# Performance work log

Measured on AMD Instinct MI355X. Metric: run time of the kernel, lower is better.

## Reference

```python
import jax, jax.numpy as jnp
import numpy as np

T, N, E = 4, 40000, 640000
D_IN, D_HID, D_OUT, NCLASS = 256, 256, 256, 2
NEG = 0.2  # leaky_relu negative slope (both GATv2 internal and outer activations)


def segment_softmax(logits, seg, n):
    m = jax.ops.segment_max(logits, seg, num_segments=n)
    ex = jnp.exp(logits - m[seg])
    s = jax.ops.segment_sum(ex, seg, num_segments=n)
    return ex / s[seg]


def gatv2(x, src, dst, Wl, Wr, bl, br, att, bias, n):
    # PyG GATv2Conv, heads=1, concat: lin_l on source, lin_r on target,
    # e = att . leaky_relu(xl_j + xr_i), softmax over incoming edges of i,
    # out_i = sum_j alpha_ij * xl_j + bias. Self-loops already appended.
    xl = x @ Wl + bl                                   # [n, C]
    xr = x @ Wr + br                                   # [n, C]
    e = jax.nn.leaky_relu(xl[src] + xr[dst], NEG)      # [E', C]
    alpha = segment_softmax(e @ att, dst, n)           # [E']
    out = jax.ops.segment_sum(alpha[:, None] * xl[src], dst, num_segments=n)
    return out + bias


def setup_inputs() -> dict:
    key = jax.random.key(0)
    ks = jax.random.split(key, 18)
    w = lambda k, shape, fan: (jax.random.normal(k, shape, dtype=jnp.float32) / np.sqrt(fan)).astype(jnp.float32)
    return {
        "fts": jax.random.normal(ks[0], (T, N, D_IN), dtype=jnp.float32),
        "graph": jax.random.randint(ks[1], (T, 2, E), 0, N, dtype=jnp.int32),
        "Wl0": w(ks[2], (D_IN, D_HID), D_IN),
        "Wr0": w(ks[3], (D_IN, D_HID), D_IN),
        "bl0": jnp.zeros((D_HID,), jnp.float32),
        "br0": jnp.zeros((D_HID,), jnp.float32),
        "att0": w(ks[4], (D_HID,), D_HID),
        "b0": jnp.zeros((D_HID,), jnp.float32),
        "Wl1": w(ks[5], (D_HID, D_OUT), D_HID),
        "Wr1": w(ks[6], (D_HID, D_OUT), D_HID),
        "bl1": jnp.zeros((D_OUT,), jnp.float32),
        "br1": jnp.zeros((D_OUT,), jnp.float32),
        "att1": w(ks[7], (D_OUT,), D_OUT),
        "b1": jnp.zeros((D_OUT,), jnp.float32),
        "W_lin": w(ks[8], (D_OUT, NCLASS), D_OUT),
        "b_lin": jnp.zeros((NCLASS,), jnp.float32),
        "time_steps": T,
    }


def reference(fts, graph, Wl0, Wr0, bl0, br0, att0, b0,
              Wl1, Wr1, bl1, br1, att1, b1, W_lin, b_lin, time_steps):
    n = fts.shape[1]
    loops = jnp.arange(n, dtype=graph.dtype)
    # PyG add_self_loops=True: append (i, i) edges per graph used.
    src0 = jnp.concatenate([graph[0, 0], loops])
    dst0 = jnp.concatenate([graph[0, 1], loops])
    # BUG-faithful: only timestep 0 survives (y = y[0]) but the last layer
    # uses G from the LAST timestep; timesteps 1..T-1 are dead compute.
    srcL = jnp.concatenate([graph[time_steps - 1, 0], loops])
    dstL = jnp.concatenate([graph[time_steps - 1, 1], loops])
    y = jax.nn.leaky_relu(gatv2(fts[0], src0, dst0, Wl0, Wr0, bl0, br0, att0, b0, n), NEG)
    y = jax.nn.leaky_relu(gatv2(y, srcL, dstL, Wl1, Wr1, bl1, br1, att1, b1, n), NEG)
    # dropout is identity in eval mode
    y = y @ W_lin + b_lin
    return jax.nn.log_softmax(y, axis=1)  # [N, nclass]
```

## Files before the change

### kernel.cpp

```cpp
#include <hip/hip_runtime.h>
#include <hip/hip_bf16.h>
#include <math.h>

#define NEG 0.2f
#define NB_MAX 256
#define CAP 5120

typedef float f32x4 __attribute__((ext_vector_type(4)));
typedef _Float16 f16;
typedef _Float16 f16x2 __attribute__((ext_vector_type(2)));
typedef _Float16 f16x8 __attribute__((ext_vector_type(8)));

#if defined(__has_builtin)
#if __has_builtin(__builtin_amdgcn_fdot2)
#define HAVE_FDOT2 1
#endif
#endif

typedef __attribute__((address_space(3))) void as3_void;
typedef __attribute__((address_space(1))) const void as1_void;

__device__ __forceinline__ void gl_lds16(const void* g, void* l) {
    __builtin_amdgcn_global_load_lds((as1_void*)g, (as3_void*)l, 16, 0, 0);
}

__global__ __launch_bounds__(256) void convert_w2(const float* __restrict__ Wl0,
                                                  const float* __restrict__ Wr0,
                                                  const float* __restrict__ Wl1,
                                                  const float* __restrict__ Wr1,
                                                  _Float16* __restrict__ Wt,
                                                  int* __restrict__ bkt_next, int nb2) {
    int l = blockIdx.y;
    int idx = blockIdx.x * blockDim.x + threadIdx.x;
    int n = idx >> 8, k = idx & 255;
    const float* Wl = l ? Wl1 : Wl0;
    const float* Wr = l ? Wr1 : Wr0;
    float v = (n < 256) ? Wl[k * 256 + n] : Wr[k * 256 + (n - 256)];
    Wt[(size_t)l * 512 * 256 + idx] = (_Float16)v;
    if (blockIdx.x == 0 && l == 0)
        for (int i = threadIdx.x; i < nb2; i += 256) bkt_next[i] = 0;
}

__device__ __forceinline__ void stage16(const _Float16* __restrict__ src,
                                        int row_base, int row_max, int k0,
                                        char* lds, int tid) {
#pragma unroll
    for (int q = 0; q < 2; ++q) {
        int off = q * 4096 + tid * 16;
        int row = off >> 6;
        int slot = (off >> 4) & 3;
        int se = slot ^ (row & 3);
        int grow = row_base + row;
        if (grow > row_max) grow = row_max;
        gl_lds16(src + (size_t)grow * 256 + k0 + se * 8,
                 lds + q * 4096 + (tid >> 6) * 1024);
    }
}

__device__ __forceinline__ void stage16_f32(const float* __restrict__ X,
                                            int row_base, int row_max, int k0,
                                            char* lds, int tid) {
#pragma unroll
    for (int u = 0; u < 4; ++u) {
        int unit = u * 256 + tid;
        int r = unit >> 3, hu = unit & 7;
        int slot = hu >> 1, sub = (hu & 1) * 8;
        int se = slot ^ (r & 3);
        int grow = row_base + r;
        if (grow > row_max) grow = row_max;
        float4 v = *(const float4*)(X + (size_t)grow * 256 + k0 + se * 8 + (hu & 1) * 4);
        f16x2 p0 = {(f16)v.x, (f16)v.y};
        f16x2 p1 = {(f16)v.z, (f16)v.w};
        uint2 w;
        w.x = __builtin_bit_cast(unsigned, p0);
        w.y = __builtin_bit_cast(unsigned, p1);
        *(uint2*)(lds + r * 64 + slot * 16 + sub) = w;
    }
}

template <int SRC>
__global__ __launch_bounds__(256) void mfma_gemm(const float* __restrict__ Xf,
                                                 const _Float16* __restrict__ X16,
                                                 const _Float16* __restrict__ Wt,
                                                 const float* __restrict__ bl,
                                                 const float* __restrict__ br,
                                                 _Float16* __restrict__ Af,
                                                 _Float16* __restrict__ Bf, int M) {
    __shared__ char smem[32768];
    int Mb = (M + 127) >> 7;
    int b = blockIdx.x;
    int cx = b & 7, rr = b >> 3;
    int m_blk = (rr >> 2) * 8 + cx;
    int n_blk = rr & 3;
    if (m_blk >= Mb) return;
    int tid = threadIdx.x;
    int wave = tid >> 6, lane = tid & 63;
    int m0 = m_blk * 128;
    int wr = wave >> 1, wc = wave & 1;
    int r15 = lane & 15, c = lane >> 4;

    f32x4 acc[4][4];
#pragma unroll
    for (int mf = 0; mf < 4; ++mf)
#pragma unroll
        for (int nf = 0; nf < 4; ++nf) acc[mf][nf] = (f32x4){0.f, 0.f, 0.f, 0.f};

    auto stageX = [&](int k0, char* dst) {
        if constexpr (SRC == 0) stage16_f32(Xf, m0, M - 1, k0, dst, tid);
        else                    stage16(X16, m0, M - 1, k0, dst, tid);
    };

    stageX(0, smem);
    stage16(Wt, n_blk * 128, 511, 0, smem + 8192, tid);
    __syncthreads();

    for (int t = 0; t < 8; ++t) {
        int buf = t & 1;
        if (t < 7) {
            char* nb = smem + (buf ^ 1) * 16384;
            stageX((t + 1) * 32, nb);
            stage16(Wt, n_blk * 128, 511, (t + 1) * 32, nb + 8192, tid);
        }
        const char* At = smem + buf * 16384;
        const char* Bt = At + 8192;
        f16x8 af[4], bf[4];
#pragma unroll
        for (int f = 0; f < 4; ++f) {
            int ar = wr * 64 + f * 16 + r15;
            af[f] = *(const f16x8*)(At + ar * 64 + ((c ^ (ar & 3)) << 4));
            int br_ = wc * 64 + f * 16 + r15;
            bf[f] = *(const f16x8*)(Bt + br_ * 64 + ((c ^ (br_ & 3)) << 4));
        }
#pragma unroll
        for (int mf = 0; mf < 4; ++mf)
#pragma unroll
            for (int nf = 0; nf < 4; ++nf)
                acc[mf][nf] = __builtin_amdgcn_mfma_f32_16x16x32_f16(af[mf], bf[nf], acc[mf][nf], 0, 0, 0);
        __syncthreads();
    }

    int q4 = (lane >> 4) * 4;
#pragma unroll
    for (int nf = 0; nf < 4; ++nf) {
        int n_abs = n_blk * 128 + wc * 64 + nf * 16 + r15;
        bool left = n_abs < 256;
        float bb = left ? bl[n_abs] : br[n_abs - 256];
        int col = n_abs & 255;
#pragma unroll
        for (int mf = 0; mf < 4; ++mf) {
            int rowb = m0 + wr * 64 + mf * 16 + q4;
#pragma unroll
            for (int j = 0; j < 4; ++j) {
                int row = rowb + j;
                if (row < M) {
                    float v = acc[mf][nf][j] + bb;
                    if (left) Af[(size_t)row * 256 + col] = (_Float16)v;
                    else      Bf[(size_t)row * 256 + col] = (_Float16)v;
                }
            }
        }
    }
}

__global__ __launch_bounds__(256) void binA(const int* __restrict__ src0,
                                            const int* __restrict__ dst0,
                                            const int* __restrict__ src1,
                                            const int* __restrict__ dst1,
                                            int Ereal, int EP, int nb,
                                            int* __restrict__ bkt_next,
                                            unsigned* __restrict__ bucketBuf) {
    __shared__ int hist[NB_MAX], base[NB_MAX], ofs[NB_MAX];
    int l = blockIdx.y;
    for (int i = threadIdx.x; i < nb; i += 256) hist[i] = 0;
    __syncthreads();
    const int* src = l ? src1 : src0;
    const int* dst = l ? dst1 : dst0;
    int c0 = blockIdx.x * 4096;
    int dcache[16];
#pragma unroll
    for (int k = 0; k < 16; ++k) {
        int i = c0 + k * 256 + threadIdx.x;
        int d = -1;
        if (i < EP) d = (i < Ereal) ? dst[i] : (i - Ereal);
        dcache[k] = d;
        if (d >= 0) atomicAdd(&hist[d >> 8], 1);
    }
    __syncthreads();
    for (int i = threadIdx.x; i < nb; i += 256) {
        base[i] = hist[i] ? atomicAdd(&bkt_next[l * nb + i], hist[i]) : 0;
        ofs[i] = 0;
    }
    __syncthreads();
#pragma unroll
    for (int k = 0; k < 16; ++k) {
        int i = c0 + k * 256 + threadIdx.x;
        int d = dcache[k];
        if (d >= 0) {
            int s = (i < Ereal) ? src[i] : (i - Ereal);
            int bk = d >> 8;
            int pos = base[bk] + atomicAdd(&ofs[bk], 1);
            bucketBuf[(size_t)(l * nb + bk) * CAP + pos] = (unsigned)s | ((unsigned)(d & 255) << 16);
        }
    }
}

__global__ __launch_bounds__(256) void binB(const unsigned* __restrict__ bucketBuf,
                                            const int* __restrict__ bkt_cnt,
                                            int nb, int N,
                                            int* __restrict__ beg,
                                            int* __restrict__ end_,
                                            int* __restrict__ csr) {
    __shared__ int hist[256], sh[256], nxt[256];
    int b = blockIdx.x, l = blockIdx.y, t = threadIdx.x;
    int cnt = bkt_cnt[l * nb + b];
    const unsigned* buf = bucketBuf + (size_t)(l * nb + b) * CAP;
    int* csrL = csr + (size_t)l * nb * CAP;
    hist[t] = 0;
    __syncthreads();
    for (int i = t; i < cnt; i += 256)
        atomicAdd(&hist[buf[i] >> 16], 1);
    __syncthreads();
    int h = hist[t];
    sh[t] = h;
    __syncthreads();
    for (int o = 1; o < 256; o <<= 1) {
        int x = (t >= o) ? sh[t - o] : 0;
        __syncthreads();
        sh[t] += x;
        __syncthreads();
    }
    int excl = sh[t] - h;
    nxt[t] = excl;
    int d = b * 256 + t;
    if (d < N) {
        beg[(size_t)l * N + d] = b * CAP + excl;
        end_[(size_t)l * N + d] = b * CAP + excl + h;
    }
    __syncthreads();
    for (int i = t; i < cnt; i += 256) {
        unsigned v = buf[i];
        int pos = b * CAP + atomicAdd(&nxt[v >> 16], 1);
        csrL[pos] = (int)(v & 0xFFFFu);
    }
}

template <int MODE>
__global__ __launch_bounds__(256) void gat_node(const _Float16* __restrict__ xl,
                                                const _Float16* __restrict__ xr,
                                                const int* __restrict__ beg_,
                                                const int* __restrict__ end_,
                                                const int* __restrict__ csr_src,
                                                const float* __restrict__ att,
                                                const float* __restrict__ bias,
                                                _Float16* __restrict__ y16,
                                                const float* __restrict__ Wlin,
                                                const float* __restrict__ blin,
                                                float* __restrict__ out, int n) {
    int wid = (int)((blockIdx.x * (size_t)blockDim.x + threadIdx.x) >> 6);
    int lane = threadIdx.x & 63;
    if (wid >= n) return;
    int g = lane >> 5, li = lane & 31;
    int beg = beg_[wid], end = end_[wid];

    f16x8 xr8 = ((const f16x8*)(xr + (size_t)wid * 256))[li];
    float4 t0 = ((const float4*)att)[li * 2];
    float4 t1 = ((const float4*)att)[li * 2 + 1];
    f16x2 t01 = {(f16)t0.x, (f16)t0.y}, t23 = {(f16)t0.z, (f16)t0.w};
    f16x2 t45 = {(f16)t1.x, (f16)t1.y}, t67 = {(f16)t1.z, (f16)t1.w};
    const f16 ng = (f16)NEG;
    const f16x8 n8 = {ng, ng, ng, ng, ng, ng, ng, ng};

    float m = -INFINITY, ssum = 0.f;
    float acc[8] = {0.f, 0.f, 0.f, 0.f, 0.f, 0.f, 0.f, 0.f};

    auto step = [&](f16x8 a, bool valid) {
        f16x8 v = a + xr8;
        f16x8 lk = __builtin_elementwise_max(v, v * n8);
#ifdef HAVE_FDOT2
        f16x2 q;
        q[0] = lk[0]; q[1] = lk[1];
        float dot = __builtin_amdgcn_fdot2(q, t01, 0.f, false);
        q[0] = lk[2]; q[1] = lk[3];
        dot = __builtin_amdgcn_fdot2(q, t23, dot, false);
        q[0] = lk[4]; q[1] = lk[5];
        dot = __builtin_amdgcn_fdot2(q, t45, dot, false);
        q[0] = lk[6]; q[1] = lk[7];
        dot = __builtin_amdgcn_fdot2(q, t67, dot, false);
#else
        float dot = (float)lk[0] * (float)t01[0] + (float)lk[1] * (float)t01[1] +
                    (float)lk[2] * (float)t23[0] + (float)lk[3] * (float)t23[1] +
                    (float)lk[4] * (float)t45[0] + (float)lk[5] * (float)t45[1] +
                    (float)lk[6] * (float)t67[0] + (float)lk[7] * (float)t67[1];
#endif
#pragma unroll
        for (int off = 16; off > 0; off >>= 1) dot += __shfl_xor(dot, off);
        if (valid) {
            if (dot > m + 8.f) {
                float sc = __expf(m - dot);
                ssum = ssum * sc + 1.f;
#pragma unroll
                for (int i = 0; i < 8; ++i) acc[i] = acc[i] * sc + (float)a[i];
                m = dot;
            } else {
                float p = __expf(dot - m);
                ssum += p;
#pragma unroll
                for (int i = 0; i < 8; ++i) acc[i] += p * (float)a[i];
            }
        }
    };

    int j = beg;
    for (; j + 16 <= end; j += 16) {
        f16x8 a[8];
#pragma unroll
        for (int u = 0; u < 8; ++u) {
            int s = csr_src[j + 2 * u + g];
            a[u] = ((const f16x8*)(xl + (size_t)s * 256))[li];
        }
#pragma unroll
        for (int u = 0; u < 8; ++u) step(a[u], true);
    }
    if (j + 8 <= end) {
        f16x8 a[4];
#pragma unroll
        for (int u = 0; u < 4; ++u) {
            int s = csr_src[j + 2 * u + g];
            a[u] = ((const f16x8*)(xl + (size_t)s * 256))[li];
        }
#pragma unroll
        for (int u = 0; u < 4; ++u) step(a[u], true);
        j += 8;
    }
    for (; j < end; j += 2) {
        int e = j + g;
        int s = csr_src[e < end ? e : end - 1];
        f16x8 a = ((const f16x8*)(xl + (size_t)s * 256))[li];
        step(a, e < end);
    }

    float m_o = __shfl_xor(m, 32);
    float s_o = __shfl_xor(ssum, 32);
    float ms = fmaxf(m, m_o);
    float wa = __expf(m - ms), wb = __expf(m_o - ms);
    float inv = 1.f / (ssum * wa + s_o * wb);
    float4 bb0 = ((const float4*)bias)[li * 2];
    float4 bb1 = ((const float4*)bias)[li * 2 + 1];
    float bbv[8] = {bb0.x, bb0.y, bb0.z, bb0.w, bb1.x, bb1.y, bb1.z, bb1.w};
    float o8[8];
#pragma unroll
    for (int i = 0; i < 8; ++i) {
        float ao = __shfl_xor(acc[i], 32);
        float o = (acc[i] * wa + ao * wb) * inv + bbv[i];
        o8[i] = o > 0.f ? o : NEG * o;
    }

    if (MODE == 0) {
        if (g == 0) {
            f16x8 w;
#pragma unroll
            for (int i = 0; i < 8; ++i) w[i] = (f16)o8[i];
            ((f16x8*)(y16 + (size_t)wid * 256))[li] = w;
        }
    } else {
        float z0 = 0.f, z1 = 0.f;
#pragma unroll
        for (int p = 0; p < 4; ++p) {
            float4 q = ((const float4*)Wlin)[li * 4 + p];
            z0 += o8[2 * p] * q.x + o8[2 * p + 1] * q.z;
            z1 += o8[2 * p] * q.y + o8[2 * p + 1] * q.w;
        }
#pragma unroll
        for (int off = 16; off > 0; off >>= 1) {
            z0 += __shfl_xor(z0, off);
            z1 += __shfl_xor(z1, off);
        }
        if (lane == 0) {
            z0 += blin[0];
            z1 += blin[1];
            float mx = fmaxf(z0, z1);
            float lse = mx + logf(expf(z0 - mx) + expf(z1 - mx));
            out[(size_t)wid * 2 + 0] = z0 - lse;
            out[(size_t)wid * 2 + 1] = z1 - lse;
        }
    }
}

extern "C" void kernel_launch(void* const* d_in, const int* in_sizes, int n_in,
                              void* d_out, int out_size, void* d_ws, size_t ws_size,
                              hipStream_t stream) {
    const float* fts   = (const float*)d_in[0];
    const int*   graph = (const int*)d_in[1];
    const float* Wl0 = (const float*)d_in[2];
    const float* Wr0 = (const float*)d_in[3];
    const float* bl0 = (const float*)d_in[4];
    const float* br0 = (const float*)d_in[5];
    const float* att0 = (const float*)d_in[6];
    const float* b0  = (const float*)d_in[7];
    const float* Wl1 = (const float*)d_in[8];
    const float* Wr1 = (const float*)d_in[9];
    const float* bl1 = (const float*)d_in[10];
    const float* br1 = (const float*)d_in[11];
    const float* att1 = (const float*)d_in[12];
    const float* b1  = (const float*)d_in[13];
    const float* Wlin = (const float*)d_in[14];
    const float* blin = (const float*)d_in[15];

    int N = out_size / 2;
    long T = in_sizes[0] / ((long)N * 256);
    long E = in_sizes[1] / (2 * T);
    int EP = (int)E + N;
    int nb = (N + 255) / 256;

    char* ws = (char*)d_ws;
    size_t off = 0;
    auto alloc = [&](size_t bytes) -> void* {
        void* p = ws + off;
        off += (bytes + 255) & ~(size_t)255;
        return p;
    };
    _Float16* Af  = (_Float16*)alloc((size_t)N * 256 * 2);
    _Float16* Bf  = (_Float16*)alloc((size_t)N * 256 * 2);
    _Float16* Y16 = (_Float16*)alloc((size_t)N * 256 * 2);
    _Float16* Wt  = (_Float16*)alloc((size_t)2 * 512 * 256 * 2);
    int* beg      = (int*)alloc((size_t)2 * N * 4);
    int* end_     = (int*)alloc((size_t)2 * N * 4);
    int* csr      = (int*)alloc((size_t)2 * nb * CAP * 4);
    unsigned* bucketBuf = (unsigned*)alloc((size_t)2 * nb * CAP * 4);
    int* bkt_next = (int*)alloc((size_t)2 * nb * 4);
    (void)ws_size; (void)n_in;

    int Mb = (N + 127) / 128;
    int gemm_blocks = ((Mb + 7) / 8) * 8 * 4;
    dim3 chunk_grid((EP + 4095) / 4096, 2);
    int node_blocks = (N + 3) / 4;

    const int* src0 = graph;
    const int* dst0 = graph + E;
    const int* srcL = graph + (T - 1) * 2 * E;
    const int* dstL = graph + (T - 1) * 2 * E + E;

    convert_w2<<<dim3(512, 2), 256, 0, stream>>>(Wl0, Wr0, Wl1, Wr1, Wt, bkt_next, 2 * nb);
    binA<<<chunk_grid, 256, 0, stream>>>(src0, dst0, srcL, dstL, (int)E, EP, nb,
                                         bkt_next, bucketBuf);
    binB<<<dim3(nb, 2), 256, 0, stream>>>(bucketBuf, bkt_next, nb, N, beg, end_, csr);

    mfma_gemm<0><<<gemm_blocks, 256, 0, stream>>>(fts, nullptr, Wt, bl0, br0, Af, Bf, N);
    gat_node<0><<<node_blocks, 256, 0, stream>>>(Af, Bf, beg, end_, csr, att0, b0,
                                                 Y16, nullptr, nullptr, nullptr, N);

    mfma_gemm<1><<<gemm_blocks, 256, 0, stream>>>(nullptr, Y16, Wt + (size_t)512 * 256,
                                                  bl1, br1, Af, Bf, N);
    gat_node<1><<<node_blocks, 256, 0, stream>>>(Af, Bf, beg + N, end_ + N,
                                                 csr + (size_t)nb * CAP, att1, b1,
                                                 nullptr, Wlin, blin, (float*)d_out, N);
}
```

Baseline: 235.1 us.

## Fuse CSR binning pass with first GEMM launch and shrink CSR indices to 16-bit

```diff
diff --git a/kernel.cpp b/kernel.cpp
--- a/kernel.cpp
+++ b/kernel.cpp
@@ -79,16 +79,15 @@
 }
 
 template <int SRC>
-__global__ __launch_bounds__(256) void mfma_gemm(const float* __restrict__ Xf,
-                                                 const _Float16* __restrict__ X16,
-                                                 const _Float16* __restrict__ Wt,
-                                                 const float* __restrict__ bl,
-                                                 const float* __restrict__ br,
-                                                 _Float16* __restrict__ Af,
-                                                 _Float16* __restrict__ Bf, int M) {
-    __shared__ char smem[32768];
+__device__ __forceinline__ void gemm_body(char* smem, int b,
+                                          const float* __restrict__ Xf,
+                                          const _Float16* __restrict__ X16,
+                                          const _Float16* __restrict__ Wt,
+                                          const float* __restrict__ bl,
+                                          const float* __restrict__ br,
+                                          _Float16* __restrict__ Af,
+                                          _Float16* __restrict__ Bf, int M) {
     int Mb = (M + 127) >> 7;
-    int b = blockIdx.x;
     int cx = b & 7, rr = b >> 3;
     int m_blk = (rr >> 2) * 8 + cx;
     int n_blk = rr & 3;
@@ -117,9 +116,9 @@
     for (int t = 0; t < 8; ++t) {
         int buf = t & 1;
         if (t < 7) {
-            char* nb = smem + (buf ^ 1) * 16384;
-            stageX((t + 1) * 32, nb);
-            stage16(Wt, n_blk * 128, 511, (t + 1) * 32, nb + 8192, tid);
+            char* nb2 = smem + (buf ^ 1) * 16384;
+            stageX((t + 1) * 32, nb2);
+            stage16(Wt, n_blk * 128, 511, (t + 1) * 32, nb2 + 8192, tid);
         }
         const char* At = smem + buf * 16384;
         const char* Bt = At + 8192;
@@ -204,44 +203,68 @@
     }
 }
 
-__global__ __launch_bounds__(256) void binB(const unsigned* __restrict__ bucketBuf,
-                                            const int* __restrict__ bkt_cnt,
-                                            int nb, int N,
-                                            int* __restrict__ beg,
-                                            int* __restrict__ end_,
-                                            int* __restrict__ csr) {
-    __shared__ int hist[256], sh[256], nxt[256];
-    int b = blockIdx.x, l = blockIdx.y, t = threadIdx.x;
-    int cnt = bkt_cnt[l * nb + b];
-    const unsigned* buf = bucketBuf + (size_t)(l * nb + b) * CAP;
-    int* csrL = csr + (size_t)l * nb * CAP;
-    hist[t] = 0;
-    __syncthreads();
-    for (int i = t; i < cnt; i += 256)
-        atomicAdd(&hist[buf[i] >> 16], 1);
-    __syncthreads();
-    int h = hist[t];
-    sh[t] = h;
-    __syncthreads();
-    for (int o = 1; o < 256; o <<= 1) {
-        int x = (t >= o) ? sh[t - o] : 0;
+__global__ __launch_bounds__(256) void binB_gemm0(const unsigned* __restrict__ bucketBuf,
+                                                  const int* __restrict__ bkt_cnt,
+                                                  int nb, int N,
+                                                  int* __restrict__ beg,
+                                                  int* __restrict__ end_,
+                                                  unsigned short* __restrict__ csr16,
+                                                  const float* __restrict__ Xf,
+                                                  const _Float16* __restrict__ Wt,
+                                                  const float* __restrict__ bl,
+                                                  const float* __restrict__ br,
+                                                  _Float16* __restrict__ Af,
+                                                  _Float16* __restrict__ Bf, int M) {
+    __shared__ char smem[32768];
+    int blk = blockIdx.x;
+    if (blk < 2 * nb) {
+        int* hist = (int*)smem;
+        int* sh   = (int*)(smem + 1024);
+        int* nxt  = (int*)(smem + 2048);
+        int l = blk / nb, b = blk % nb, t = threadIdx.x;
+        int cnt = bkt_cnt[l * nb + b];
+        const unsigned* buf = bucketBuf + (size_t)(l * nb + b) * CAP;
+        unsigned short* csrL = csr16 + (size_t)l * nb * CAP;
+        hist[t] = 0;
         __syncthreads();
-        sh[t] += x;
+        for (int i = t; i < cnt; i += 256)
+            atomicAdd(&hist[buf[i] >> 16], 1);
         __syncthreads();
-    }
-    int excl = sh[t] - h;
-    nxt[t] = excl;
-    int d = b * 256 + t;
-    if (d < N) {
-        beg[(size_t)l * N + d] = b * CAP + excl;
-        end_[(size_t)l * N + d] = b * CAP + excl + h;
-    }
-    __syncthreads();
-    for (int i = t; i < cnt; i += 256) {
-        unsigned v = buf[i];
-        int pos = b * CAP + atomicAdd(&nxt[v >> 16], 1);
-        csrL[pos] = (int)(v & 0xFFFFu);
-    }
+        int h = hist[t];
+        sh[t] = h;
+        __syncthreads();
+        for (int o = 1; o < 256; o <<= 1) {
+            int x = (t >= o) ? sh[t - o] : 0;
+            __syncthreads();
+            sh[t] += x;
+            __syncthreads();
+        }
+        int excl = sh[t] - h;
+        nxt[t] = excl;
+        int d = b * 256 + t;
+        if (d < N) {
+            beg[(size_t)l * N + d] = b * CAP + excl;
+            end_[(size_t)l * N + d] = b * CAP + excl + h;
+        }
+        __syncthreads();
+        for (int i = t; i < cnt; i += 256) {
+            unsigned v = buf[i];
+            int pos = b * CAP + atomicAdd(&nxt[v >> 16], 1);
+            csrL[pos] = (unsigned short)(v & 0xFFFFu);
+        }
+        return;
+    }
+    gemm_body<0>(smem, blk - 2 * nb, Xf, nullptr, Wt, bl, br, Af, Bf, M);
+}
+
+__global__ __launch_bounds__(256) void mfma_gemm1(const _Float16* __restrict__ X16,
+                                                  const _Float16* __restrict__ Wt,
+                                                  const float* __restrict__ bl,
+                                                  const float* __restrict__ br,
+                                                  _Float16* __restrict__ Af,
+                                                  _Float16* __restrict__ Bf, int M) {
+    __shared__ char smem[32768];
+    gemm_body<1>(smem, blockIdx.x, nullptr, X16, Wt, bl, br, Af, Bf, M);
 }
 
 template <int MODE>
@@ -249,7 +272,7 @@
                                                 const _Float16* __restrict__ xr,
                                                 const int* __restrict__ beg_,
                                                 const int* __restrict__ end_,
-                                                const int* __restrict__ csr_src,
+                                                const unsigned short* __restrict__ csr,
                                                 const float* __restrict__ att,
                                                 const float* __restrict__ bias,
                                                 _Float16* __restrict__ y16,
@@ -315,7 +338,7 @@
         f16x8 a[8];
 #pragma unroll
         for (int u = 0; u < 8; ++u) {
-            int s = csr_src[j + 2 * u + g];
+            int s = csr[j + 2 * u + g];
             a[u] = ((const f16x8*)(xl + (size_t)s * 256))[li];
         }
 #pragma unroll
@@ -325,7 +348,7 @@
         f16x8 a[4];
 #pragma unroll
         for (int u = 0; u < 4; ++u) {
-            int s = csr_src[j + 2 * u + g];
+            int s = csr[j + 2 * u + g];
             a[u] = ((const f16x8*)(xl + (size_t)s * 256))[li];
         }
 #pragma unroll
@@ -334,7 +357,7 @@
     }
     for (; j < end; j += 2) {
         int e = j + g;
-        int s = csr_src[e < end ? e : end - 1];
+        int s = csr[e < end ? e : end - 1];
         f16x8 a = ((const f16x8*)(xl + (size_t)s * 256))[li];
         step(a, e < end);
     }
@@ -425,7 +448,7 @@
     _Float16* Wt  = (_Float16*)alloc((size_t)2 * 512 * 256 * 2);
     int* beg      = (int*)alloc((size_t)2 * N * 4);
     int* end_     = (int*)alloc((size_t)2 * N * 4);
-    int* csr      = (int*)alloc((size_t)2 * nb * CAP * 4);
+    unsigned short* csr16 = (unsigned short*)alloc((size_t)2 * nb * CAP * 2);
     unsigned* bucketBuf = (unsigned*)alloc((size_t)2 * nb * CAP * 4);
     int* bkt_next = (int*)alloc((size_t)2 * nb * 4);
     (void)ws_size; (void)n_in;
@@ -443,15 +466,14 @@
     convert_w2<<<dim3(512, 2), 256, 0, stream>>>(Wl0, Wr0, Wl1, Wr1, Wt, bkt_next, 2 * nb);
     binA<<<chunk_grid, 256, 0, stream>>>(src0, dst0, srcL, dstL, (int)E, EP, nb,
                                          bkt_next, bucketBuf);
-    binB<<<dim3(nb, 2), 256, 0, stream>>>(bucketBuf, bkt_next, nb, N, beg, end_, csr);
-
-    mfma_gemm<0><<<gemm_blocks, 256, 0, stream>>>(fts, nullptr, Wt, bl0, br0, Af, Bf, N);
-    gat_node<0><<<node_blocks, 256, 0, stream>>>(Af, Bf, beg, end_, csr, att0, b0,
+    binB_gemm0<<<2 * nb + gemm_blocks, 256, 0, stream>>>(bucketBuf, bkt_next, nb, N,
+                                                         beg, end_, csr16,
+                                                         fts, Wt, bl0, br0, Af, Bf, N);
+    gat_node<0><<<node_blocks, 256, 0, stream>>>(Af, Bf, beg, end_, csr16, att0, b0,
                                                  Y16, nullptr, nullptr, nullptr, N);
-
-    mfma_gemm<1><<<gemm_blocks, 256, 0, stream>>>(nullptr, Y16, Wt + (size_t)512 * 256,
-                                                  bl1, br1, Af, Bf, N);
+    mfma_gemm1<<<gemm_blocks, 256, 0, stream>>>(Y16, Wt + (size_t)512 * 256,
+                                                bl1, br1, Af, Bf, N);
     gat_node<1><<<node_blocks, 256, 0, stream>>>(Af, Bf, beg + N, end_ + N,
-                                                 csr + (size_t)nb * CAP, att1, b1,
+                                                 csr16 + (size_t)nb * CAP, att1, b1,
                                                  nullptr, Wlin, blin, (float*)d_out, N);
 }
```

New measurement: 232.6 us. Within noise of the previous version (-1.1%).
